# Optimization experiments

Hardware: AMD Instinct MI355X
Metric: run time of the kernel (lower is better)

The kernel has to match this reference:

```python
import jax, jax.numpy as jnp
import numpy as np

NUM_EXPERTS = 8
TOP_K = 2
D_MODEL = 1024
D_MLP = 3584
BATCH, POS = 2, 2048


def setup_inputs() -> dict:
    key = jax.random.key(0)
    ks = jax.random.split(key, 5)
    scale = 0.02
    x = jax.random.normal(ks[0], (BATCH, POS, D_MODEL), dtype=jnp.float32)
    W_gate = jax.random.normal(ks[1], (NUM_EXPERTS, D_MODEL), dtype=jnp.float32) * scale
    W1 = jax.random.normal(ks[2], (NUM_EXPERTS, D_MLP, D_MODEL), dtype=jnp.float32) * scale
    W3 = jax.random.normal(ks[3], (NUM_EXPERTS, D_MLP, D_MODEL), dtype=jnp.float32) * scale
    W2 = jax.random.normal(ks[4], (NUM_EXPERTS, D_MODEL, D_MLP), dtype=jnp.float32) * scale
    return {"x": x, "W_gate": W_gate, "W1": W1, "W3": W3, "W2": W2}


def reference(x, W_gate, W1, W3, W2):
    batch, pos, d_model = x.shape
    xt = x.reshape(-1, d_model)                      # [T, d]
    T = xt.shape[0]

    # --- top-2 softmax gating ---
    gate_logits = xt @ W_gate.T                      # [T, E]
    weights = jax.nn.softmax(gate_logits.astype(jnp.float32), axis=-1)
    top_w, top_i = jax.lax.top_k(weights, TOP_K)     # [T, k]
    top_w = top_w / jnp.sum(top_w, axis=-1, keepdims=True)
    top_w = top_w.astype(gate_logits.dtype)

    # dense combine weights: zero for non-selected experts  [T, E]
    combine = jnp.zeros((T, NUM_EXPERTS), dtype=xt.dtype)
    combine = combine.at[jnp.arange(T)[:, None], top_i].set(top_w)

    # --- per-expert SwiGLU MLP, computed dense over all tokens ---
    h1 = jnp.einsum('td,efd->etf', xt, W1)           # [E, T, ffn]
    h3 = jnp.einsum('td,efd->etf', xt, W3)           # [E, T, ffn]
    h = jax.nn.silu(h1) * h3                         # [E, T, ffn]
    expert_out = jnp.einsum('etf,edf->etd', h, W2)   # [E, T, d]

    # --- weighted combine ---
    out = jnp.einsum('etd,te->td', expert_out, combine)  # [T, d]
    return out.reshape(batch, pos, d_model)
```

## Files before the change

kernel.cpp:

```cpp
#include <hip/hip_runtime.h>
#include <hip/hip_bf16.h>
#include <math.h>


#define NUM_EXPERTS 8
#define TOPK 2
#define D_MODEL 1024
#define D_MLP 3584
#define T_TOKENS 4096
#define NSLOT (T_TOKENS * TOPK)
#define SLOT_CAP 9216

#define BM 128
#define BN 128
#define BK 32
#define LDT 40

typedef __attribute__((ext_vector_type(8))) short bf16x8;
typedef __attribute__((ext_vector_type(4))) float f32x4;

#define WS_SMALL 147456
#define H_BYTES ((size_t)SLOT_CAP * D_MLP * 2)
#define XB_OFF (WS_SMALL + H_BYTES)
#define XB_BYTES ((size_t)T_TOKENS * D_MODEL * 2)
#define W1B_OFF (XB_OFF + XB_BYTES)
#define W13_BYTES ((size_t)NUM_EXPERTS * (size_t)D_MLP * D_MODEL * 2)
#define W3B_OFF (W1B_OFF + W13_BYTES)
#define WS_FULL (W3B_OFF + W13_BYTES)
#define W2B_OFF WS_FULL
#define WS_BIG (W2B_OFF + W13_BYTES)
#define WS_NEEDED_OLD (WS_SMALL + H_BYTES)

#define NW8 (NUM_EXPERTS * D_MLP * D_MODEL / 8)

__device__ inline unsigned short f32_to_bf16(float f) {
  union { float f; unsigned int u; } v; v.f = f;
  unsigned int u = v.u;
  unsigned int r = (u + 0x7FFFu + ((u >> 16) & 1u)) >> 16;
  return (unsigned short)r;
}

__device__ inline bf16x8 pack8(float4 a, float4 b) {
  bf16x8 v;
  v[0] = (short)f32_to_bf16(a.x); v[1] = (short)f32_to_bf16(a.y);
  v[2] = (short)f32_to_bf16(a.z); v[3] = (short)f32_to_bf16(a.w);
  v[4] = (short)f32_to_bf16(b.x); v[5] = (short)f32_to_bf16(b.y);
  v[6] = (short)f32_to_bf16(b.z); v[7] = (short)f32_to_bf16(b.w);
  return v;
}

__device__ __forceinline__ void gload16(const void* g, void* l) {
  __builtin_amdgcn_global_load_lds(
      (__attribute__((address_space(1))) void*)g,
      (__attribute__((address_space(3))) void*)l, 16, 0, 0);
}

__global__ void zero_kernel(float4* __restrict__ p, int n4) {
  int i = blockIdx.x * blockDim.x + threadIdx.x;
  if (i < n4) p[i] = make_float4(0.f, 0.f, 0.f, 0.f);
}

__global__ __launch_bounds__(256) void cvt_kernel(const float* __restrict__ src,
                                                  unsigned short* __restrict__ dst,
                                                  int n8) {
  int i = blockIdx.x * blockDim.x + threadIdx.x;
  const int stride = gridDim.x * blockDim.x;
  for (; i < n8; i += stride) {
    const float4* s = (const float4*)(src + (size_t)i * 8);
    float4 a = s[0], b = s[1];
    *(bf16x8*)(dst + (size_t)i * 8) = pack8(a, b);
  }
}

__global__ __launch_bounds__(64) void gate_kernel(const float* __restrict__ x,
                            const float* __restrict__ Wg,
                            int* __restrict__ top_idx,
                            float* __restrict__ top_w,
                            unsigned short* __restrict__ Xb) {
  const int t = blockIdx.x;
  const int lane = threadIdx.x;
  const float* xr = x + (size_t)t * D_MODEL;

  float xs[16];
#pragma unroll
  for (int i = 0; i < 16; ++i) xs[i] = xr[lane + i * 64];

  if (Xb) {
    const float4* xr4 = (const float4*)(xr + lane * 16);
    float4 a0 = xr4[0], a1 = xr4[1], a2 = xr4[2], a3 = xr4[3];
    unsigned short* xbrow = Xb + (size_t)t * D_MODEL + lane * 16;
    *(bf16x8*)(xbrow) = pack8(a0, a1);
    *(bf16x8*)(xbrow + 8) = pack8(a2, a3);
  }

  float logits[NUM_EXPERTS];
#pragma unroll
  for (int e = 0; e < NUM_EXPERTS; ++e) {
    const float* wr = Wg + (size_t)e * D_MODEL;
    float s = 0.f;
#pragma unroll
    for (int i = 0; i < 16; ++i) s += xs[i] * wr[lane + i * 64];
    for (int o = 32; o > 0; o >>= 1) s += __shfl_down(s, o);
    logits[e] = s;
  }

  if (lane == 0) {
    int i0 = 0;
#pragma unroll
    for (int e = 1; e < NUM_EXPERTS; ++e)
      if (logits[e] > logits[i0]) i0 = e;
    int i1 = -1;
#pragma unroll
    for (int e = 0; e < NUM_EXPERTS; ++e) {
      if (e == i0) continue;
      if (i1 < 0 || logits[e] > logits[i1]) i1 = e;
    }
    float w0 = 1.0f / (1.0f + expf(logits[i1] - logits[i0]));
    top_idx[2 * t] = i0; top_idx[2 * t + 1] = i1;
    top_w[2 * t] = w0;   top_w[2 * t + 1] = 1.0f - w0;
  }
}

__global__ __launch_bounds__(256) void route_cvt_kernel(
    int* __restrict__ top_idx,
    const float* __restrict__ top_w,
    int* __restrict__ hdr,
    int* __restrict__ slot_token,
    float* __restrict__ slot_weight,
    const float* __restrict__ W1,
    const float* __restrict__ W3,
    unsigned short* __restrict__ W1b,
    unsigned short* __restrict__ W3b) {
  const int tid = threadIdx.x;
  if (blockIdx.x != 0) {
    const int wid = blockIdx.x - 1;
    const int stride = (gridDim.x - 1) * 256;
    for (int i = wid * 256 + tid; i < NW8; i += stride) {
      const float4* s = (const float4*)(W1 + (size_t)i * 8);
      float4 a = s[0], b = s[1];
      *(bf16x8*)(W1b + (size_t)i * 8) = pack8(a, b);
    }
    for (int i = wid * 256 + tid; i < NW8; i += stride) {
      const float4* s = (const float4*)(W3 + (size_t)i * 8);
      float4 a = s[0], b = s[1];
      *(bf16x8*)(W3b + (size_t)i * 8) = pack8(a, b);
    }
    return;
  }
  __shared__ int cnt[NUM_EXPERTS];
  __shared__ int off[NUM_EXPERTS];
  __shared__ int cur[NUM_EXPERTS];
  if (tid < NUM_EXPERTS) cnt[tid] = 0;
  __syncthreads();
  for (int k = tid; k < NSLOT; k += 256) atomicAdd(&cnt[top_idx[k]], 1);
  __syncthreads();
  if (tid == 0) {
    int o = 0;
    for (int e = 0; e < NUM_EXPERTS; ++e) {
      off[e] = o;
      int p = (cnt[e] + BM - 1) & ~(BM - 1);
      hdr[e] = cnt[e];
      hdr[8 + e] = o;
      hdr[16 + e] = p;
      o += p;
    }
  }
  __syncthreads();
  if (tid < NUM_EXPERTS) cur[tid] = off[tid];
  for (int i = tid; i < SLOT_CAP; i += 256) { slot_token[i] = 0; slot_weight[i] = 0.0f; }
  __syncthreads();
  for (int k = tid; k < NSLOT; k += 256) {
    int e = top_idx[k];
    int p = atomicAdd(&cur[e], 1);
    slot_token[p] = k >> 1;
    slot_weight[p] = top_w[k];
    top_idx[k] = p;
  }
}

__global__ __launch_bounds__(256) void gemm1_p(
    const unsigned short* __restrict__ Xb,
    const unsigned short* __restrict__ W1b,
    const unsigned short* __restrict__ W3b,
    const int* __restrict__ hdr,
    const int* __restrict__ slot_token,
    unsigned short* __restrict__ H,
    const float* __restrict__ W2src,
    unsigned short* __restrict__ W2dst) {
  if (blockIdx.z == NUM_EXPERTS) {
    const int wid = blockIdx.y * gridDim.x + blockIdx.x;
    const int stride = gridDim.x * gridDim.y * 256;
    for (int i = wid * 256 + threadIdx.x; i < NW8; i += stride) {
      const float4* s = (const float4*)(W2src + (size_t)i * 8);
      float4 a = s[0], b = s[1];
      *(bf16x8*)(W2dst + (size_t)i * 8) = pack8(a, b);
    }
    return;
  }
  const int e = blockIdx.z;
  const int pad_cnt = hdr[16 + e];
  const int m0 = blockIdx.y * BM;
  if (m0 >= pad_cnt) return;
  const int base = hdr[8 + e];
  const int n0 = blockIdx.x * BN;

  __shared__ unsigned short As[2][BM * BK];
  __shared__ unsigned short B1s[2][BN * BK];
  __shared__ unsigned short B3s[2][BN * BK];

  const int tid = threadIdx.x;
  const int lane = tid & 63;
  const int wave = tid >> 6;
  const int wm = (wave >> 1) * 64;
  const int wn = (wave & 1) * 64;
  const int l15 = lane & 15;
  const int quad = lane >> 4;

  const int r0 = tid >> 2;
  const int cc = (tid & 3) * 8;
  const int tokA0 = slot_token[base + m0 + r0];
  const int tokA1 = slot_token[base + m0 + 64 + r0];
  const unsigned short* gA0 = Xb + (size_t)tokA0 * D_MODEL + cc;
  const unsigned short* gA1 = Xb + (size_t)tokA1 * D_MODEL + cc;
  const unsigned short* gB1_0 = W1b + ((size_t)e * D_MLP + n0 + r0) * D_MODEL + cc;
  const unsigned short* gB1_1 = gB1_0 + (size_t)64 * D_MODEL;
  const unsigned short* gB3_0 = W3b + ((size_t)e * D_MLP + n0 + r0) * D_MODEL + cc;
  const unsigned short* gB3_1 = gB3_0 + (size_t)64 * D_MODEL;
  const int wb = wave * 512;

  const f32x4 fzero = {0.f, 0.f, 0.f, 0.f};
  f32x4 acc1[4][4], acc3[4][4];
#pragma unroll
  for (int i = 0; i < 4; ++i)
#pragma unroll
    for (int j = 0; j < 4; ++j) { acc1[i][j] = fzero; acc3[i][j] = fzero; }

#define NT1 (D_MODEL / BK)
  gload16(gA0, &As[0][wb]);
  gload16(gA1, &As[0][2048 + wb]);
  gload16(gB1_0, &B1s[0][wb]);
  gload16(gB1_1, &B1s[0][2048 + wb]);
  gload16(gB3_0, &B3s[0][wb]);
  gload16(gB3_1, &B3s[0][2048 + wb]);
  asm volatile("s_waitcnt vmcnt(0)" ::: "memory");
  __builtin_amdgcn_s_barrier();
  asm volatile("" ::: "memory");

#pragma unroll
  for (int t = 0; t < NT1; ++t) {
    const int p = t & 1;
    if (t + 1 < NT1) {
      const int q = p ^ 1;
      const int k1 = (t + 1) * BK;
      gload16(gA0 + k1, &As[q][wb]);
      gload16(gA1 + k1, &As[q][2048 + wb]);
      gload16(gB1_0 + k1, &B1s[q][wb]);
      gload16(gB1_1 + k1, &B1s[q][2048 + wb]);
      gload16(gB3_0 + k1, &B3s[q][wb]);
      gload16(gB3_1 + k1, &B3s[q][2048 + wb]);
    }
    bf16x8 af[4], b1f[4], b3f[4];
#pragma unroll
    for (int i = 0; i < 4; ++i)
      af[i] = *(const bf16x8*)(&As[p][(wm + i * 16 + l15) * BK + quad * 8]);
#pragma unroll
    for (int j = 0; j < 4; ++j) {
      b1f[j] = *(const bf16x8*)(&B1s[p][(wn + j * 16 + l15) * BK + quad * 8]);
      b3f[j] = *(const bf16x8*)(&B3s[p][(wn + j * 16 + l15) * BK + quad * 8]);
    }
#pragma unroll
    for (int i = 0; i < 4; ++i)
#pragma unroll
      for (int j = 0; j < 4; ++j) {
        acc1[i][j] = __builtin_amdgcn_mfma_f32_16x16x32_bf16(af[i], b1f[j], acc1[i][j], 0, 0, 0);
        acc3[i][j] = __builtin_amdgcn_mfma_f32_16x16x32_bf16(af[i], b3f[j], acc3[i][j], 0, 0, 0);
      }
    if (t + 1 < NT1) {
      asm volatile("s_waitcnt vmcnt(0)" ::: "memory");
      __builtin_amdgcn_s_barrier();
      asm volatile("" ::: "memory");
    }
  }

  const size_t hbase = (size_t)(base + m0);
#pragma unroll
  for (int i = 0; i < 4; ++i) {
    const int mrow = wm + i * 16 + quad * 4;
#pragma unroll
    for (int r = 0; r < 4; ++r) {
      unsigned short* hrow = H + (hbase + mrow + r) * D_MLP + n0;
#pragma unroll
      for (int j = 0; j < 4; ++j) {
        float h1 = acc1[i][j][r];
        float h3 = acc3[i][j][r];
        float s = h1 / (1.0f + __expf(-h1));
        hrow[wn + j * 16 + l15] = f32_to_bf16(s * h3);
      }
    }
  }
}

__global__ __launch_bounds__(256) void gemm2_p(
    const unsigned short* __restrict__ H,
    const unsigned short* __restrict__ W2b,
    const int* __restrict__ hdr,
    float* __restrict__ Y) {
  const int e = blockIdx.z;
  const int pad_cnt = hdr[16 + e];
  const int m0 = blockIdx.y * BM;
  if (m0 >= pad_cnt) return;
  const int base = hdr[8 + e];
  const int n0 = blockIdx.x * BN;

  __shared__ unsigned short As[2][BM * BK];
  __shared__ unsigned short Bs[2][BN * BK];

  const int tid = threadIdx.x;
  const int lane = tid & 63;
  const int wave = tid >> 6;
  const int wm = (wave >> 1) * 64;
  const int wn = (wave & 1) * 64;
  const int l15 = lane & 15;
  const int quad = lane >> 4;

  const int r0 = tid >> 2;
  const int cc = (tid & 3) * 8;
  const unsigned short* gA0 = H + (size_t)(base + m0 + r0) * D_MLP + cc;
  const unsigned short* gA1 = gA0 + (size_t)64 * D_MLP;
  const unsigned short* gB0 = W2b + ((size_t)e * D_MODEL + n0 + r0) * D_MLP + cc;
  const unsigned short* gB1 = gB0 + (size_t)64 * D_MLP;
  const int wb = wave * 512;

  const f32x4 fzero = {0.f, 0.f, 0.f, 0.f};
  f32x4 acc[4][4];
#pragma unroll
  for (int i = 0; i < 4; ++i)
#pragma unroll
    for (int j = 0; j < 4; ++j) acc[i][j] = fzero;

#define NT2 (D_MLP / BK)
  gload16(gA0, &As[0][wb]);
  gload16(gA1, &As[0][2048 + wb]);
  gload16(gB0, &Bs[0][wb]);
  gload16(gB1, &Bs[0][2048 + wb]);
  asm volatile("s_waitcnt vmcnt(0)" ::: "memory");
  __builtin_amdgcn_s_barrier();
  asm volatile("" ::: "memory");

#pragma unroll 2
  for (int t = 0; t < NT2; ++t) {
    const int p = t & 1;
    if (t + 1 < NT2) {
      const int q = p ^ 1;
      const int k1 = (t + 1) * BK;
      gload16(gA0 + k1, &As[q][wb]);
      gload16(gA1 + k1, &As[q][2048 + wb]);
      gload16(gB0 + k1, &Bs[q][wb]);
      gload16(gB1 + k1, &Bs[q][2048 + wb]);
    }
    bf16x8 af[4], bf[4];
#pragma unroll
    for (int i = 0; i < 4; ++i)
      af[i] = *(const bf16x8*)(&As[p][(wm + i * 16 + l15) * BK + quad * 8]);
#pragma unroll
    for (int j = 0; j < 4; ++j)
      bf[j] = *(const bf16x8*)(&Bs[p][(wn + j * 16 + l15) * BK + quad * 8]);
#pragma unroll
    for (int i = 0; i < 4; ++i)
#pragma unroll
      for (int j = 0; j < 4; ++j)
        acc[i][j] = __builtin_amdgcn_mfma_f32_16x16x32_bf16(af[i], bf[j], acc[i][j], 0, 0, 0);
    if (t + 1 < NT2) {
      asm volatile("s_waitcnt vmcnt(0)" ::: "memory");
      __builtin_amdgcn_s_barrier();
      asm volatile("" ::: "memory");
    }
  }

#pragma unroll
  for (int i = 0; i < 4; ++i) {
    const int mrow = wm + i * 16 + quad * 4;
#pragma unroll
    for (int r = 0; r < 4; ++r) {
      float* yrow = Y + (size_t)(base + m0 + mrow + r) * D_MODEL + n0;
#pragma unroll
      for (int j = 0; j < 4; ++j)
        yrow[wn + j * 16 + l15] = acc[i][j][r];
    }
  }
}

__global__ __launch_bounds__(256) void combine_kernel(
    const float* __restrict__ Y,
    const int* __restrict__ slot_of,
    const float* __restrict__ top_w,
    float* __restrict__ out) {
  const int t = blockIdx.x;
  const int c = threadIdx.x;
  const int p0 = slot_of[2 * t], p1 = slot_of[2 * t + 1];
  const float w0 = top_w[2 * t], w1 = top_w[2 * t + 1];
  const float4 y0 = ((const float4*)(Y + (size_t)p0 * D_MODEL))[c];
  const float4 y1 = ((const float4*)(Y + (size_t)p1 * D_MODEL))[c];
  float4 o;
  o.x = w0 * y0.x + w1 * y1.x;
  o.y = w0 * y0.y + w1 * y1.y;
  o.z = w0 * y0.z + w1 * y1.z;
  o.w = w0 * y0.w + w1 * y1.w;
  ((float4*)(out + (size_t)t * D_MODEL))[c] = o;
}


__global__ __launch_bounds__(256) void gemm1_kernel(const float* __restrict__ x,
                             const float* __restrict__ W1,
                             const float* __restrict__ W3,
                             const int* __restrict__ hdr,
                             const int* __restrict__ slot_token,
                             unsigned short* __restrict__ H) {
  const int e = blockIdx.z;
  const int pad_cnt = hdr[16 + e];
  const int m0 = blockIdx.y * BM;
  if (m0 >= pad_cnt) return;
  const int base = hdr[8 + e];
  const int n0 = blockIdx.x * BN;

  __shared__ unsigned short As[BM * LDT];
  __shared__ unsigned short B1s[BN * LDT];
  __shared__ unsigned short B3s[BN * LDT];

  const int tid = threadIdx.x;
  const int lane = tid & 63;
  const int wave = tid >> 6;
  const int wm = (wave >> 1) * 64;
  const int wn = (wave & 1) * 64;
  const int l15 = lane & 15;
  const int quad = lane >> 4;

  const int sr = tid >> 1;
  const int sc = (tid & 1) * 16;
  const float* arow = x + (size_t)slot_token[base + m0 + sr] * D_MODEL + sc;
  const float* b1row = W1 + ((size_t)e * D_MLP + n0 + sr) * D_MODEL + sc;
  const float* b3row = W3 + ((size_t)e * D_MLP + n0 + sr) * D_MODEL + sc;

  const f32x4 fzero = {0.f, 0.f, 0.f, 0.f};
  f32x4 acc1[4][4], acc3[4][4];
#pragma unroll
  for (int i = 0; i < 4; ++i)
#pragma unroll
    for (int j = 0; j < 4; ++j) { acc1[i][j] = fzero; acc3[i][j] = fzero; }

  for (int k0 = 0; k0 < D_MODEL; k0 += BK) {
    const float4* ap = (const float4*)(arow + k0);
    const float4* b1p = (const float4*)(b1row + k0);
    const float4* b3p = (const float4*)(b3row + k0);
    float4 a0 = ap[0], a1 = ap[1], a2 = ap[2], a3 = ap[3];
    float4 c0 = b1p[0], c1 = b1p[1], c2 = b1p[2], c3 = b1p[3];
    float4 d0 = b3p[0], d1 = b3p[1], d2 = b3p[2], d3 = b3p[3];
    __syncthreads();
    *(bf16x8*)(&As[sr * LDT + sc]) = pack8(a0, a1);
    *(bf16x8*)(&As[sr * LDT + sc + 8]) = pack8(a2, a3);
    *(bf16x8*)(&B1s[sr * LDT + sc]) = pack8(c0, c1);
    *(bf16x8*)(&B1s[sr * LDT + sc + 8]) = pack8(c2, c3);
    *(bf16x8*)(&B3s[sr * LDT + sc]) = pack8(d0, d1);
    *(bf16x8*)(&B3s[sr * LDT + sc + 8]) = pack8(d2, d3);
    __syncthreads();

    bf16x8 a_frag[4], b1_frag[4], b3_frag[4];
#pragma unroll
    for (int i = 0; i < 4; ++i)
      a_frag[i] = *(const bf16x8*)(&As[(wm + i * 16 + l15) * LDT + quad * 8]);
#pragma unroll
    for (int j = 0; j < 4; ++j) {
      b1_frag[j] = *(const bf16x8*)(&B1s[(wn + j * 16 + l15) * LDT + quad * 8]);
      b3_frag[j] = *(const bf16x8*)(&B3s[(wn + j * 16 + l15) * LDT + quad * 8]);
    }
#pragma unroll
    for (int i = 0; i < 4; ++i)
#pragma unroll
      for (int j = 0; j < 4; ++j) {
        acc1[i][j] = __builtin_amdgcn_mfma_f32_16x16x32_bf16(a_frag[i], b1_frag[j], acc1[i][j], 0, 0, 0);
        acc3[i][j] = __builtin_amdgcn_mfma_f32_16x16x32_bf16(a_frag[i], b3_frag[j], acc3[i][j], 0, 0, 0);
      }
  }

  const size_t hbase = (size_t)(base + m0);
#pragma unroll
  for (int i = 0; i < 4; ++i) {
    const int mrow = wm + i * 16 + quad * 4;
#pragma unroll
    for (int r = 0; r < 4; ++r) {
      unsigned short* hrow = H + (hbase + mrow + r) * D_MLP + n0;
#pragma unroll
      for (int j = 0; j < 4; ++j) {
        float h1 = acc1[i][j][r];
        float h3 = acc3[i][j][r];
        float s = h1 / (1.0f + __expf(-h1));
        hrow[wn + j * 16 + l15] = f32_to_bf16(s * h3);
      }
    }
  }
}

__global__ __launch_bounds__(256) void gemm2_kernel(const unsigned short* __restrict__ H,
                             const float* __restrict__ W2,
                             const int* __restrict__ hdr,
                             const int* __restrict__ slot_token,
                             const float* __restrict__ slot_weight,
                             float* __restrict__ out) {
  const int e = blockIdx.z;
  const int pad_cnt = hdr[16 + e];
  const int m0 = blockIdx.y * BM;
  if (m0 >= pad_cnt) return;
  const int base = hdr[8 + e];
  const int n0 = blockIdx.x * BN;

  __shared__ unsigned short As[BM * LDT];
  __shared__ unsigned short Bs[BN * LDT];

  const int tid = threadIdx.x;
  const int lane = tid & 63;
  const int wave = tid >> 6;
  const int wm = (wave >> 1) * 64;
  const int wn = (wave & 1) * 64;
  const int l15 = lane & 15;
  const int quad = lane >> 4;

  const int sr = tid >> 1;
  const int sc = (tid & 1) * 16;
  const unsigned short* arow = H + (size_t)(base + m0 + sr) * D_MLP + sc;
  const float* brow = W2 + ((size_t)e * D_MODEL + n0 + sr) * D_MLP + sc;

  const f32x4 fzero = {0.f, 0.f, 0.f, 0.f};
  f32x4 acc[4][4];
#pragma unroll
  for (int i = 0; i < 4; ++i)
#pragma unroll
    for (int j = 0; j < 4; ++j) acc[i][j] = fzero;

  for (int k0 = 0; k0 < D_MLP; k0 += BK) {
    const uint4* ap = (const uint4*)(arow + k0);
    uint4 a0 = ap[0], a1 = ap[1];
    const float4* bp = (const float4*)(brow + k0);
    float4 c0 = bp[0], c1 = bp[1], c2 = bp[2], c3 = bp[3];
    __syncthreads();
    *(uint4*)(&As[sr * LDT + sc]) = a0;
    *(uint4*)(&As[sr * LDT + sc + 8]) = a1;
    *(bf16x8*)(&Bs[sr * LDT + sc]) = pack8(c0, c1);
    *(bf16x8*)(&Bs[sr * LDT + sc + 8]) = pack8(c2, c3);
    __syncthreads();

    bf16x8 a_frag[4], b_frag[4];
#pragma unroll
    for (int i = 0; i < 4; ++i)
      a_frag[i] = *(const bf16x8*)(&As[(wm + i * 16 + l15) * LDT + quad * 8]);
#pragma unroll
    for (int j = 0; j < 4; ++j)
      b_frag[j] = *(const bf16x8*)(&Bs[(wn + j * 16 + l15) * LDT + quad * 8]);
#pragma unroll
    for (int i = 0; i < 4; ++i)
#pragma unroll
      for (int j = 0; j < 4; ++j)
        acc[i][j] = __builtin_amdgcn_mfma_f32_16x16x32_bf16(a_frag[i], b_frag[j], acc[i][j], 0, 0, 0);
  }

#pragma unroll
  for (int i = 0; i < 4; ++i) {
    const int mrow = wm + i * 16 + quad * 4;
#pragma unroll
    for (int r = 0; r < 4; ++r) {
      const int srow = base + m0 + mrow + r;
      const float w = slot_weight[srow];
      if (w != 0.0f) {
        const int tok = slot_token[srow];
        float* orow = out + (size_t)tok * D_MODEL + n0;
#pragma unroll
        for (int j = 0; j < 4; ++j)
          atomicAdd(&orow[wn + j * 16 + l15], acc[i][j][r] * w);
      }
    }
  }
}

extern "C" void kernel_launch(void* const* d_in, const int* in_sizes, int n_in,
                              void* d_out, int out_size, void* d_ws, size_t ws_size,
                              hipStream_t stream) {
  const float* x  = (const float*)d_in[0];
  const float* Wg = (const float*)d_in[1];
  const float* W1 = (const float*)d_in[2];
  const float* W3 = (const float*)d_in[3];
  const float* W2 = (const float*)d_in[4];
  float* out = (float*)d_out;

  if (ws_size < WS_NEEDED_OLD) return;

  char* ws = (char*)d_ws;
  int*   top_idx     = (int*)(ws);
  float* top_w       = (float*)(ws + 32768);
  int*   hdr         = (int*)(ws + 65536);
  int*   slot_token  = (int*)(ws + 65792);
  float* slot_weight = (float*)(ws + 102656);
  unsigned short* H  = (unsigned short*)(ws + WS_SMALL);

  if (ws_size >= WS_FULL) {
    unsigned short* Xb  = (unsigned short*)(ws + XB_OFF);
    unsigned short* W1b = (unsigned short*)(ws + W1B_OFF);
    unsigned short* W3b = (unsigned short*)(ws + W3B_OFF);
    float* Y = (float*)(ws + W3B_OFF);
    const bool big = (ws_size >= WS_BIG);
    unsigned short* W2b = big ? (unsigned short*)(ws + W2B_OFF)
                              : W1b;

    gate_kernel<<<T_TOKENS, 64, 0, stream>>>(x, Wg, top_idx, top_w, Xb);
    route_cvt_kernel<<<2049, 256, 0, stream>>>(top_idx, top_w, hdr, slot_token,
                                               slot_weight, W1, W3, W1b, W3b);
    if (big) {
      gemm1_p<<<dim3(D_MLP / BN, T_TOKENS / BM, NUM_EXPERTS + 1), 256, 0, stream>>>(
          Xb, W1b, W3b, hdr, slot_token, H, W2, W2b);
    } else {
      gemm1_p<<<dim3(D_MLP / BN, T_TOKENS / BM, NUM_EXPERTS), 256, 0, stream>>>(
          Xb, W1b, W3b, hdr, slot_token, H, nullptr, nullptr);
      cvt_kernel<<<2048, 256, 0, stream>>>(W2, W2b, NW8);
    }
    gemm2_p<<<dim3(D_MODEL / BN, T_TOKENS / BM, NUM_EXPERTS), 256, 0, stream>>>(
        H, W2b, hdr, Y);
    combine_kernel<<<T_TOKENS, 256, 0, stream>>>(Y, top_idx, top_w, out);
  } else {
    gate_kernel<<<T_TOKENS, 64, 0, stream>>>(x, Wg, top_idx, top_w, nullptr);
    route_cvt_kernel<<<1, 256, 0, stream>>>(top_idx, top_w, hdr, slot_token,
                                            slot_weight, nullptr, nullptr,
                                            nullptr, nullptr);
    zero_kernel<<<(out_size / 4 + 255) / 256, 256, 0, stream>>>((float4*)d_out, out_size / 4);
    gemm1_kernel<<<dim3(D_MLP / BN, T_TOKENS / BM, NUM_EXPERTS), 256, 0, stream>>>(
        x, W1, W3, hdr, slot_token, H);
    gemm2_kernel<<<dim3(D_MODEL / BN, T_TOKENS / BM, NUM_EXPERTS), 256, 0, stream>>>(
        H, W2, hdr, slot_token, slot_weight, out);
  }
}
```

Measured before the change: 711.8 us.

## Move W2 conversion into routing kernel and restructure GEMM wait/barrier pipeline

The W2 fp32-to-bf16 conversion moves out of the extra z-slice of gemm1 and into the route/convert kernel, next to the W1/W3 conversion. Both grouped GEMMs change their double-buffer sync. Each iteration now issues the next tile's loads, then waits only for the older loads (vmcnt of 6 or 4) before a barrier, with a second barrier after the MFMAs. The aim is to overlap global loads with compute and to stop the W2 conversion from sharing gemm1's grid. In exchange there is an extra barrier per iteration, and W2 conversion now runs serially before gemm1 instead of alongside it.

```diff
diff --git a/kernel.cpp b/kernel.cpp
--- a/kernel.cpp
+++ b/kernel.cpp
@@ -129,8 +129,10 @@
     float* __restrict__ slot_weight,
     const float* __restrict__ W1,
     const float* __restrict__ W3,
+    const float* __restrict__ W2,
     unsigned short* __restrict__ W1b,
-    unsigned short* __restrict__ W3b) {
+    unsigned short* __restrict__ W3b,
+    unsigned short* __restrict__ W2b) {
   const int tid = threadIdx.x;
   if (blockIdx.x != 0) {
     const int wid = blockIdx.x - 1;
@@ -144,6 +146,13 @@
       const float4* s = (const float4*)(W3 + (size_t)i * 8);
       float4 a = s[0], b = s[1];
       *(bf16x8*)(W3b + (size_t)i * 8) = pack8(a, b);
+    }
+    if (W2) {
+      for (int i = wid * 256 + tid; i < NW8; i += stride) {
+        const float4* s = (const float4*)(W2 + (size_t)i * 8);
+        float4 a = s[0], b = s[1];
+        *(bf16x8*)(W2b + (size_t)i * 8) = pack8(a, b);
+      }
     }
     return;
   }
@@ -184,19 +193,7 @@
     const unsigned short* __restrict__ W3b,
     const int* __restrict__ hdr,
     const int* __restrict__ slot_token,
-    unsigned short* __restrict__ H,
-    const float* __restrict__ W2src,
-    unsigned short* __restrict__ W2dst) {
-  if (blockIdx.z == NUM_EXPERTS) {
-    const int wid = blockIdx.y * gridDim.x + blockIdx.x;
-    const int stride = gridDim.x * gridDim.y * 256;
-    for (int i = wid * 256 + threadIdx.x; i < NW8; i += stride) {
-      const float4* s = (const float4*)(W2src + (size_t)i * 8);
-      float4 a = s[0], b = s[1];
-      *(bf16x8*)(W2dst + (size_t)i * 8) = pack8(a, b);
-    }
-    return;
-  }
+    unsigned short* __restrict__ H) {
   const int e = blockIdx.z;
   const int pad_cnt = hdr[16 + e];
   const int m0 = blockIdx.y * BM;
@@ -242,15 +239,12 @@
   gload16(gB1_1, &B1s[0][2048 + wb]);
   gload16(gB3_0, &B3s[0][wb]);
   gload16(gB3_1, &B3s[0][2048 + wb]);
-  asm volatile("s_waitcnt vmcnt(0)" ::: "memory");
-  __builtin_amdgcn_s_barrier();
-  asm volatile("" ::: "memory");
 
 #pragma unroll
   for (int t = 0; t < NT1; ++t) {
     const int p = t & 1;
     if (t + 1 < NT1) {
-      const int q = p ^ 1;
+      const int q = (t + 1) & 1;
       const int k1 = (t + 1) * BK;
       gload16(gA0 + k1, &As[q][wb]);
       gload16(gA1 + k1, &As[q][2048 + wb]);
@@ -258,7 +252,13 @@
       gload16(gB1_1 + k1, &B1s[q][2048 + wb]);
       gload16(gB3_0 + k1, &B3s[q][wb]);
       gload16(gB3_1 + k1, &B3s[q][2048 + wb]);
-    }
+      asm volatile("s_waitcnt vmcnt(6)" ::: "memory");
+    } else {
+      asm volatile("s_waitcnt vmcnt(0)" ::: "memory");
+    }
+    __builtin_amdgcn_s_barrier();
+    asm volatile("" ::: "memory");
+
     bf16x8 af[4], b1f[4], b3f[4];
 #pragma unroll
     for (int i = 0; i < 4; ++i)
@@ -275,11 +275,8 @@
         acc1[i][j] = __builtin_amdgcn_mfma_f32_16x16x32_bf16(af[i], b1f[j], acc1[i][j], 0, 0, 0);
         acc3[i][j] = __builtin_amdgcn_mfma_f32_16x16x32_bf16(af[i], b3f[j], acc3[i][j], 0, 0, 0);
       }
-    if (t + 1 < NT1) {
-      asm volatile("s_waitcnt vmcnt(0)" ::: "memory");
-      __builtin_amdgcn_s_barrier();
-      asm volatile("" ::: "memory");
-    }
+    asm volatile("" ::: "memory");
+    __builtin_amdgcn_s_barrier();
   }
 
   const size_t hbase = (size_t)(base + m0);
@@ -343,21 +340,24 @@
   gload16(gA1, &As[0][2048 + wb]);
   gload16(gB0, &Bs[0][wb]);
   gload16(gB1, &Bs[0][2048 + wb]);
-  asm volatile("s_waitcnt vmcnt(0)" ::: "memory");
-  __builtin_amdgcn_s_barrier();
-  asm volatile("" ::: "memory");
 
 #pragma unroll 2
   for (int t = 0; t < NT2; ++t) {
     const int p = t & 1;
     if (t + 1 < NT2) {
-      const int q = p ^ 1;
+      const int q = (t + 1) & 1;
       const int k1 = (t + 1) * BK;
       gload16(gA0 + k1, &As[q][wb]);
       gload16(gA1 + k1, &As[q][2048 + wb]);
       gload16(gB0 + k1, &Bs[q][wb]);
       gload16(gB1 + k1, &Bs[q][2048 + wb]);
-    }
+      asm volatile("s_waitcnt vmcnt(4)" ::: "memory");
+    } else {
+      asm volatile("s_waitcnt vmcnt(0)" ::: "memory");
+    }
+    __builtin_amdgcn_s_barrier();
+    asm volatile("" ::: "memory");
+
     bf16x8 af[4], bf[4];
 #pragma unroll
     for (int i = 0; i < 4; ++i)
@@ -370,11 +370,8 @@
 #pragma unroll
       for (int j = 0; j < 4; ++j)
         acc[i][j] = __builtin_amdgcn_mfma_f32_16x16x32_bf16(af[i], bf[j], acc[i][j], 0, 0, 0);
-    if (t + 1 < NT2) {
-      asm volatile("s_waitcnt vmcnt(0)" ::: "memory");
-      __builtin_amdgcn_s_barrier();
-      asm volatile("" ::: "memory");
-    }
+    asm volatile("" ::: "memory");
+    __builtin_amdgcn_s_barrier();
   }
 
 #pragma unroll
@@ -610,24 +607,20 @@
                               : W1b;
 
     gate_kernel<<<T_TOKENS, 64, 0, stream>>>(x, Wg, top_idx, top_w, Xb);
-    route_cvt_kernel<<<2049, 256, 0, stream>>>(top_idx, top_w, hdr, slot_token,
-                                               slot_weight, W1, W3, W1b, W3b);
-    if (big) {
-      gemm1_p<<<dim3(D_MLP / BN, T_TOKENS / BM, NUM_EXPERTS + 1), 256, 0, stream>>>(
-          Xb, W1b, W3b, hdr, slot_token, H, W2, W2b);
-    } else {
-      gemm1_p<<<dim3(D_MLP / BN, T_TOKENS / BM, NUM_EXPERTS), 256, 0, stream>>>(
-          Xb, W1b, W3b, hdr, slot_token, H, nullptr, nullptr);
-      cvt_kernel<<<2048, 256, 0, stream>>>(W2, W2b, NW8);
-    }
+    route_cvt_kernel<<<2049, 256, 0, stream>>>(
+        top_idx, top_w, hdr, slot_token, slot_weight,
+        W1, W3, big ? W2 : nullptr, W1b, W3b, W2b);
+    gemm1_p<<<dim3(D_MLP / BN, T_TOKENS / BM, NUM_EXPERTS), 256, 0, stream>>>(
+        Xb, W1b, W3b, hdr, slot_token, H);
+    if (!big) cvt_kernel<<<2048, 256, 0, stream>>>(W2, W2b, NW8);
     gemm2_p<<<dim3(D_MODEL / BN, T_TOKENS / BM, NUM_EXPERTS), 256, 0, stream>>>(
         H, W2b, hdr, Y);
     combine_kernel<<<T_TOKENS, 256, 0, stream>>>(Y, top_idx, top_w, out);
   } else {
     gate_kernel<<<T_TOKENS, 64, 0, stream>>>(x, Wg, top_idx, top_w, nullptr);
-    route_cvt_kernel<<<1, 256, 0, stream>>>(top_idx, top_w, hdr, slot_token,
-                                            slot_weight, nullptr, nullptr,
-                                            nullptr, nullptr);
+    route_cvt_kernel<<<1, 256, 0, stream>>>(
+        top_idx, top_w, hdr, slot_token, slot_weight,
+        nullptr, nullptr, nullptr, nullptr, nullptr, nullptr);
     zero_kernel<<<(out_size / 4 + 255) / 256, 256, 0, stream>>>((float4*)d_out, out_size / 4);
     gemm1_kernel<<<dim3(D_MLP / BN, T_TOKENS / BM, NUM_EXPERTS), 256, 0, stream>>>(
         x, W1, W3, hdr, slot_token, H);
```

Result: faster. 630.9 us (-11.4%).
